# Kernel optimization log

Measured on AMD Instinct MI355X. Metric: run time of the kernel, lower is better.

## Reference

```python
import jax, jax.numpy as jnp
import numpy as np

EMB = 256
N = 262144
B = 512
SLOPE = 0.01  # torch LeakyReLU default negative slope


def leaky_relu(x):
    return jnp.where(x >= 0, x, SLOPE * x)


def setup_inputs() -> dict:
    key = jax.random.key(0)
    ks = jax.random.split(key, 10)
    s = 1.0 / np.sqrt(EMB)
    s2 = 1.0 / np.sqrt(2 * EMB)
    return {
        "xg_prev": jax.random.normal(ks[0], (B, EMB), jnp.float32),
        "x": jax.random.normal(ks[1], (N, EMB), jnp.float32),
        "batch_ind": jnp.sort(jax.random.randint(ks[2], (N,), 0, B)),
        "W_mask": jax.random.uniform(ks[3], (EMB, 1), jnp.float32, -s, s),
        "b_mask": jax.random.uniform(ks[4], (1,), jnp.float32, -s, s),
        "W_feat": jax.random.uniform(ks[5], (EMB, EMB), jnp.float32, -s, s),
        "b_feat": jax.random.uniform(ks[6], (EMB,), jnp.float32, -s, s),
        "W_t": jax.random.uniform(ks[7], (2 * EMB, EMB), jnp.float32, -s2, s2),
        "b_t": jax.random.uniform(ks[8], (EMB,), jnp.float32, -s2, s2),
    }


def reference(xg_prev, x, batch_ind, W_mask, b_mask, W_feat, b_feat, W_t, b_t):
    # GlobalAttention pooling (PyG): gate = att_mask(x), feat = att_feat(x)
    gate = (x @ W_mask + b_mask)[:, 0]                      # [N]
    feat = leaky_relu(x @ W_feat + b_feat)                  # [N, EMB]
    # segment-wise stable softmax over gate per graph
    seg_max = jax.ops.segment_max(gate, batch_ind, num_segments=B)  # [B]
    seg_max = jnp.where(jnp.isfinite(seg_max), seg_max, 0.0)
    e = jnp.exp(gate - seg_max[batch_ind])                  # [N]
    denom = jax.ops.segment_sum(e, batch_ind, num_segments=B)      # [B]
    w = e / jnp.maximum(denom[batch_ind], 1e-16)            # [N]
    xg = jax.ops.segment_sum(w[:, None] * feat, batch_ind, num_segments=B)  # [B, EMB]
    # concat -> linear -> leaky_relu -> residual
    h = jnp.concatenate([xg, xg_prev], axis=1)              # [B, 2*EMB]
    out = leaky_relu(h @ W_t + b_t) + xg_prev               # [B, EMB]
    return out
```

## Files before the change

### kernel.cpp

```cpp
#include <hip/hip_runtime.h>
#include <cstdint>
#include <cstddef>

#define NROWS 262144
#define EMB 256
#define NB 512
#define NCOPY 8
#define SLOPE 0.01f

typedef __attribute__((ext_vector_type(8))) short short8;
typedef __attribute__((ext_vector_type(4))) float f32x4;

__device__ __forceinline__ unsigned short f2bf(float f) {
    unsigned u = __float_as_uint(f);
    u += 0x7FFFu + ((u >> 16) & 1u);
    return (unsigned short)(u >> 16);
}

__device__ __forceinline__ short8 pack8(const float4& lo, const float4& hi) {
    short8 s;
    s[0] = (short)f2bf(lo.x); s[1] = (short)f2bf(lo.y);
    s[2] = (short)f2bf(lo.z); s[3] = (short)f2bf(lo.w);
    s[4] = (short)f2bf(hi.x); s[5] = (short)f2bf(hi.y);
    s[6] = (short)f2bf(hi.z); s[7] = (short)f2bf(hi.w);
    return s;
}

__device__ __forceinline__ void gld16u(unsigned short* l, const unsigned short* g) {
    __builtin_amdgcn_global_load_lds(
        (const __attribute__((address_space(1))) unsigned int*)g,
        (__attribute__((address_space(3))) unsigned int*)l, 16, 0, 0);
}

__global__ __launch_bounds__(256) void k_init(float4* xgPart4, float4* dPart4) {
    int i = blockIdx.x * 256 + threadIdx.x;
    if (i < NCOPY * NB * EMB / 4) xgPart4[i] = (float4){0.f, 0.f, 0.f, 0.f};
    else dPart4[i - NCOPY * NB * EMB / 4] = (float4){0.f, 0.f, 0.f, 0.f};
}

__global__ __launch_bounds__(256) void k_prep(const float* __restrict__ Wf,
                                              unsigned short* __restrict__ Wt2) {
    int b = blockIdx.x, t = threadIdx.x;
    float v = Wf[(size_t)b * EMB + t];
    Wt2[((size_t)(b >> 3) << 11) + (t << 3) + (b & 7)] = f2bf(v);
}

#define STAGE_B(B, KT) do {                                                       \
    _Pragma("unroll")                                                             \
    for (int q = 0; q < 2; q++) {                                                 \
        const int i_ = q * 512 + t;                                               \
        const int slab_ = i_ >> 8, off_ = i_ & 255;                               \
        gld16u(&bbuf[B][slab_ * 2048 + off_ * 8],                                 \
               Wt2 + (((size_t)((KT) >> 3) + slab_) << 11) + off_ * 8);           \
    }                                                                             \
} while (0)

__global__ __launch_bounds__(512, 6) void k_fused(const float* __restrict__ x,
                                                  const unsigned short* __restrict__ Wt2,
                                                  const float* __restrict__ wm,
                                                  const float* __restrict__ bfeat,
                                                  const int* __restrict__ bind,
                                                  float* __restrict__ dPart,
                                                  float* __restrict__ xgPart) {
    __shared__ unsigned short bbuf[2][32 * 256];
    __shared__ float wm_s[256];
    __shared__ float w_s[64];
    __shared__ float pxg[2][256];
    __shared__ float pden[2];
    __shared__ int   seg_s[64];
    __shared__ int   segid_s[4];
    __shared__ int   uni_s[4];

    const int t    = threadIdx.x;
    const int lane = t & 63;
    const int w    = t >> 6;
    const int wr   = w >> 1, wc = w & 1;
    const int fr   = lane & 15;
    const int fg   = lane >> 4;
    const size_t r0 = (size_t)blockIdx.x * 64;
    const int cp   = blockIdx.x & (NCOPY - 1);

    if (t < 256) { wm_s[t] = wm[t]; pxg[0][t] = 0.f; pxg[1][t] = 0.f; }
    if (t < 64) seg_s[t] = bind[r0 + t];
    if (t < 2)  pden[t] = 0.f;

    const float* xrow = x + (r0 + wr * 16 + fr) * EMB + fg * 8;

    STAGE_B(0, 0);
    float4 aLo = *reinterpret_cast<const float4*>(xrow);
    float4 aHi = *reinterpret_cast<const float4*>(xrow + 4);

    f32x4 acc[8];
#pragma unroll
    for (int n = 0; n < 8; n++) acc[n] = (f32x4){0.f, 0.f, 0.f, 0.f};
    float gp = 0.f;

#pragma unroll
    for (int s = 0; s < 8; s++) {
        const int buf = s & 1;
        float4 nLo, nHi;
        if (s < 7) {
            STAGE_B(buf ^ 1, (s + 1) * 32);
            nLo = *reinterpret_cast<const float4*>(xrow + (s + 1) * 32);
            nHi = *reinterpret_cast<const float4*>(xrow + (s + 1) * 32 + 4);
        }
        if (s < 7) asm volatile("s_waitcnt vmcnt(6)" ::: "memory");
        else       asm volatile("s_waitcnt vmcnt(0)" ::: "memory");
        __builtin_amdgcn_sched_barrier(0);
        __builtin_amdgcn_s_barrier();
        __builtin_amdgcn_sched_barrier(0);

        const float4 wa  = *reinterpret_cast<const float4*>(&wm_s[s * 32 + fg * 8]);
        const float4 wbv = *reinterpret_cast<const float4*>(&wm_s[s * 32 + fg * 8 + 4]);
        gp += aLo.x * wa.x + aLo.y * wa.y + aLo.z * wa.z + aLo.w * wa.w
            + aHi.x * wbv.x + aHi.y * wbv.y + aHi.z * wbv.z + aHi.w * wbv.w;
        const short8 a = pack8(aLo, aHi);
        const unsigned short* bb = &bbuf[buf][0];
#pragma unroll
        for (int n = 0; n < 8; n++) {
            const short8 b = *reinterpret_cast<const short8*>(
                &bb[fg * 2048 + ((wc * 128 + n * 16 + fr) << 3)]);
            acc[n] = __builtin_amdgcn_mfma_f32_16x16x32_bf16(a, b, acc[n], 0, 0, 0);
        }

        asm volatile("s_waitcnt lgkmcnt(0)" ::: "memory");
        __builtin_amdgcn_sched_barrier(0);
        __builtin_amdgcn_s_barrier();
        __builtin_amdgcn_sched_barrier(0);

        aLo = nLo; aHi = nHi;
    }

    gp += __shfl_xor(gp, 16, 64);
    gp += __shfl_xor(gp, 32, 64);
    if (wc == 0 && lane < 16) w_s[wr * 16 + lane] = expf(gp);
    if (t < 4) {
        int s0 = seg_s[t * 16], ok = 1;
#pragma unroll
        for (int i = 1; i < 16; i++) ok &= (seg_s[t * 16 + i] == s0);
        segid_s[t] = s0;
        uni_s[t]   = ok;
    }
    __syncthreads();

    const int sid0 = seg_s[0];
    const int sid1 = seg_s[63];

    if (t < 4) {
        if (uni_s[t]) {
            float s = 0.f;
#pragma unroll
            for (int i = 0; i < 16; i++) s += w_s[t * 16 + i];
            const int sid = segid_s[t];
            if (sid == sid0)      atomicAdd(&pden[0], s);
            else if (sid == sid1) atomicAdd(&pden[1], s);
            else atomicAdd(&dPart[cp * NB + sid], s);
        } else {
            for (int i = 0; i < 16; i++) {
                const int sd = seg_s[t * 16 + i];
                const float e = w_s[t * 16 + i];
                if (sd == sid0)      atomicAdd(&pden[0], e);
                else if (sd == sid1) atomicAdd(&pden[1], e);
                else atomicAdd(&dPart[cp * NB + sd], e);
            }
        }
    }

    {
        const int g    = wr;
        const int uni  = uni_s[g];
        const int sid  = segid_s[g];
        const int rowb = wr * 16;
#pragma unroll
        for (int n = 0; n < 8; n++) {
            const int col = wc * 128 + n * 16 + fr;
            const float bia = bfeat[col];
            float vr[4];
#pragma unroll
            for (int r = 0; r < 4; r++) {
                const int row = rowb + fg * 4 + r;
                float v = acc[n][r] + bia;
                v = (v >= 0.f) ? v : SLOPE * v;
                vr[r] = v * w_s[row];
            }
            if (uni) {
                float s = vr[0] + vr[1] + vr[2] + vr[3];
                s += __shfl_xor(s, 16, 64);
                s += __shfl_xor(s, 32, 64);
                if (fg == 0) {
                    if (sid == sid0)      atomicAdd(&pxg[0][col], s);
                    else if (sid == sid1) atomicAdd(&pxg[1][col], s);
                    else atomicAdd(&xgPart[((size_t)(cp * NB + sid) << 8) + col], s);
                }
            } else {
#pragma unroll
                for (int r = 0; r < 4; r++) {
                    const int sd = seg_s[rowb + fg * 4 + r];
                    if (sd == sid0)      atomicAdd(&pxg[0][col], vr[r]);
                    else if (sd == sid1) atomicAdd(&pxg[1][col], vr[r]);
                    else atomicAdd(&xgPart[((size_t)(cp * NB + sd) << 8) + col], vr[r]);
                }
            }
        }
    }
    __syncthreads();

    if (t < 256) {
        atomicAdd(&xgPart[((size_t)(cp * NB + sid0) << 8) + t], pxg[0][t]);
    } else if (sid1 != sid0) {
        atomicAdd(&xgPart[((size_t)(cp * NB + sid1) << 8) + (t - 256)], pxg[1][t - 256]);
    }
    if (t == 0) atomicAdd(&dPart[cp * NB + sid0], pden[0]);
    if (t == 1 && sid1 != sid0) atomicAdd(&dPart[cp * NB + sid1], pden[1]);
}

__global__ __launch_bounds__(256) void k_out(const float* __restrict__ xgPart,
                                             const float* __restrict__ dPart,
                                             const float* __restrict__ xgp,
                                             const float* __restrict__ Wtr,
                                             const float* __restrict__ bt,
                                             float* __restrict__ out) {
    __shared__ float h[8][512];
    const int c  = threadIdx.x;
    const int b0 = blockIdx.x * 8;
#pragma unroll
    for (int r = 0; r < 8; r++) {
        const int b = b0 + r;
        float den = 0.f, s = 0.f;
#pragma unroll
        for (int cpy = 0; cpy < NCOPY; cpy++) {
            den += dPart[cpy * NB + b];
            s   += xgPart[((size_t)(cpy * NB + b) << 8) + c];
        }
        h[r][c]       = s / fmaxf(den, 1e-16f);
        h[r][EMB + c] = xgp[(size_t)b * EMB + c];
    }
    __syncthreads();
    float acc[8] = {0.f, 0.f, 0.f, 0.f, 0.f, 0.f, 0.f, 0.f};
    for (int k = 0; k < 2 * EMB; k++) {
        float wv = Wtr[(size_t)k * EMB + c];
#pragma unroll
        for (int r = 0; r < 8; r++) acc[r] += h[r][k] * wv;
    }
#pragma unroll
    for (int r = 0; r < 8; r++) {
        float v = acc[r] + bt[c];
        v = (v >= 0.f) ? v : SLOPE * v;
        out[(size_t)(b0 + r) * EMB + c] = v + xgp[(size_t)(b0 + r) * EMB + c];
    }
}

extern "C" void kernel_launch(void* const* d_in, const int* in_sizes, int n_in,
                              void* d_out, int out_size, void* d_ws, size_t ws_size,
                              hipStream_t stream) {
    const float* xgp  = (const float*)d_in[0];
    const float* x    = (const float*)d_in[1];
    const int*   bind = (const int*)d_in[2];
    const float* Wm   = (const float*)d_in[3];
    const float* Wf   = (const float*)d_in[5];
    const float* bf   = (const float*)d_in[6];
    const float* Wtr  = (const float*)d_in[7];
    const float* bt   = (const float*)d_in[8];
    float* out = (float*)d_out;

    char* ws = (char*)d_ws;
    unsigned short* Wt2    = (unsigned short*)ws;
    float*          dPart  = (float*)(ws + 131072);
    float*          xgPart = (float*)(ws + 131072 + 16384);

    hipLaunchKernelGGL(k_init,  dim3(1028),       dim3(256), 0, stream,
                       (float4*)xgPart, (float4*)dPart);
    hipLaunchKernelGGL(k_prep,  dim3(256),        dim3(256), 0, stream, Wf, Wt2);
    hipLaunchKernelGGL(k_fused, dim3(NROWS / 64), dim3(512), 0, stream,
                       x, Wt2, Wm, bf, bind, dPart, xgPart);
    hipLaunchKernelGGL(k_out,   dim3(NB / 8),     dim3(256), 0, stream,
                       xgPart, dPart, xgp, Wtr, bt, out);
}
```

Before: 161.3 us.

## Stage x tiles into LDS via async global_load_lds and merge init into prep

The main kernel now loads x through async global-to-LDS copies into a double-buffered, XOR-swizzled shared tile instead of direct register loads. Each thread then reads its A fragment from LDS. This is meant to overlap x loads with MFMA work and cut VGPR pressure. It costs 16KB of extra LDS per block, which may lower occupancy. Separately, the zeroing kernel is folded into the weight-prep kernel to save one launch.

```diff
diff --git a/kernel.cpp b/kernel.cpp
--- a/kernel.cpp
+++ b/kernel.cpp
@@ -26,26 +26,38 @@
     return s;
 }
 
+__device__ __forceinline__ void gld16f(float* l, const float* g) {
+    __builtin_amdgcn_global_load_lds(
+        (const __attribute__((address_space(1))) unsigned int*)g,
+        (__attribute__((address_space(3))) unsigned int*)l, 16, 0, 0);
+}
 __device__ __forceinline__ void gld16u(unsigned short* l, const unsigned short* g) {
     __builtin_amdgcn_global_load_lds(
         (const __attribute__((address_space(1))) unsigned int*)g,
         (__attribute__((address_space(3))) unsigned int*)l, 16, 0, 0);
 }
 
-__global__ __launch_bounds__(256) void k_init(float4* xgPart4, float4* dPart4) {
-    int i = blockIdx.x * 256 + threadIdx.x;
-    if (i < NCOPY * NB * EMB / 4) xgPart4[i] = (float4){0.f, 0.f, 0.f, 0.f};
-    else dPart4[i - NCOPY * NB * EMB / 4] = (float4){0.f, 0.f, 0.f, 0.f};
-}
-
 __global__ __launch_bounds__(256) void k_prep(const float* __restrict__ Wf,
-                                              unsigned short* __restrict__ Wt2) {
-    int b = blockIdx.x, t = threadIdx.x;
-    float v = Wf[(size_t)b * EMB + t];
-    Wt2[((size_t)(b >> 3) << 11) + (t << 3) + (b & 7)] = f2bf(v);
-}
-
-#define STAGE_B(B, KT) do {                                                       \
+                                              unsigned short* __restrict__ Wt2,
+                                              float4* __restrict__ xgPart4,
+                                              float4* __restrict__ dPart4) {
+    const int b = blockIdx.x, t = threadIdx.x;
+    if (b < 256) {
+        float v = Wf[(size_t)b * EMB + t];
+        Wt2[((size_t)(b >> 3) << 11) + (t << 3) + (b & 7)] = f2bf(v);
+    } else {
+        const int i = (b - 256) * 256 + t;
+        if (i < NCOPY * NB * EMB / 4) xgPart4[i] = (float4){0.f, 0.f, 0.f, 0.f};
+        else dPart4[i - NCOPY * NB * EMB / 4] = (float4){0.f, 0.f, 0.f, 0.f};
+    }
+}
+
+#define STAGE(B, KT) do {                                                         \
+    {                                                                             \
+        const int row_ = t >> 3, c_ = t & 7;                                      \
+        const int cs_ = c_ ^ (row_ & 7);                                          \
+        gld16f(&xbuf[B][t * 4], x + ((r0 + row_) << 8) + (KT) + (cs_ << 2));      \
+    }                                                                             \
     _Pragma("unroll")                                                             \
     for (int q = 0; q < 2; q++) {                                                 \
         const int i_ = q * 512 + t;                                               \
@@ -62,6 +74,7 @@
                                                   const int* __restrict__ bind,
                                                   float* __restrict__ dPart,
                                                   float* __restrict__ xgPart) {
+    __shared__ float          xbuf[2][64 * 32];
     __shared__ unsigned short bbuf[2][32 * 256];
     __shared__ float wm_s[256];
     __shared__ float w_s[64];
@@ -84,11 +97,7 @@
     if (t < 64) seg_s[t] = bind[r0 + t];
     if (t < 2)  pden[t] = 0.f;
 
-    const float* xrow = x + (r0 + wr * 16 + fr) * EMB + fg * 8;
-
-    STAGE_B(0, 0);
-    float4 aLo = *reinterpret_cast<const float4*>(xrow);
-    float4 aHi = *reinterpret_cast<const float4*>(xrow + 4);
+    STAGE(0, 0);
 
     f32x4 acc[8];
 #pragma unroll
@@ -98,24 +107,26 @@
 #pragma unroll
     for (int s = 0; s < 8; s++) {
         const int buf = s & 1;
-        float4 nLo, nHi;
-        if (s < 7) {
-            STAGE_B(buf ^ 1, (s + 1) * 32);
-            nLo = *reinterpret_cast<const float4*>(xrow + (s + 1) * 32);
-            nHi = *reinterpret_cast<const float4*>(xrow + (s + 1) * 32 + 4);
-        }
-        if (s < 7) asm volatile("s_waitcnt vmcnt(6)" ::: "memory");
-        else       asm volatile("s_waitcnt vmcnt(0)" ::: "memory");
+        if (s < 7) STAGE(buf ^ 1, (s + 1) * 32);
+        if (s == 0)     asm volatile("s_waitcnt vmcnt(3) lgkmcnt(0)" ::: "memory");
+        else if (s < 7) asm volatile("s_waitcnt vmcnt(3)" ::: "memory");
+        else            asm volatile("s_waitcnt vmcnt(0)" ::: "memory");
         __builtin_amdgcn_sched_barrier(0);
         __builtin_amdgcn_s_barrier();
         __builtin_amdgcn_sched_barrier(0);
+
+        const float* xb = &xbuf[buf][0];
+        const unsigned short* bb = &bbuf[buf][0];
 
         const float4 wa  = *reinterpret_cast<const float4*>(&wm_s[s * 32 + fg * 8]);
         const float4 wbv = *reinterpret_cast<const float4*>(&wm_s[s * 32 + fg * 8 + 4]);
-        gp += aLo.x * wa.x + aLo.y * wa.y + aLo.z * wa.z + aLo.w * wa.w
-            + aHi.x * wbv.x + aHi.y * wbv.y + aHi.z * wbv.z + aHi.w * wbv.w;
-        const short8 a = pack8(aLo, aHi);
-        const unsigned short* bb = &bbuf[buf][0];
+        const int r  = wr * 16 + fr;
+        const int sl = (fg * 2) ^ (r & 7);
+        const float4 lo = *reinterpret_cast<const float4*>(&xb[r * 32 + sl * 4]);
+        const float4 hi = *reinterpret_cast<const float4*>(&xb[r * 32 + (sl ^ 1) * 4]);
+        gp += lo.x * wa.x + lo.y * wa.y + lo.z * wa.z + lo.w * wa.w
+            + hi.x * wbv.x + hi.y * wbv.y + hi.z * wbv.z + hi.w * wbv.w;
+        const short8 a = pack8(lo, hi);
 #pragma unroll
         for (int n = 0; n < 8; n++) {
             const short8 b = *reinterpret_cast<const short8*>(
@@ -127,8 +138,6 @@
         __builtin_amdgcn_sched_barrier(0);
         __builtin_amdgcn_s_barrier();
         __builtin_amdgcn_sched_barrier(0);
-
-        aLo = nLo; aHi = nHi;
     }
 
     gp += __shfl_xor(gp, 16, 64);
@@ -167,9 +176,8 @@
     }
 
     {
-        const int g    = wr;
-        const int uni  = uni_s[g];
-        const int sid  = segid_s[g];
+        const int uni  = uni_s[wr];
+        const int sid  = segid_s[wr];
         const int rowb = wr * 16;
 #pragma unroll
         for (int n = 0; n < 8; n++) {
@@ -177,11 +185,11 @@
             const float bia = bfeat[col];
             float vr[4];
 #pragma unroll
-            for (int r = 0; r < 4; r++) {
-                const int row = rowb + fg * 4 + r;
-                float v = acc[n][r] + bia;
+            for (int r2 = 0; r2 < 4; r2++) {
+                const int row = rowb + fg * 4 + r2;
+                float v = acc[n][r2] + bia;
                 v = (v >= 0.f) ? v : SLOPE * v;
-                vr[r] = v * w_s[row];
+                vr[r2] = v * w_s[row];
             }
             if (uni) {
                 float s = vr[0] + vr[1] + vr[2] + vr[3];
@@ -194,11 +202,11 @@
                 }
             } else {
 #pragma unroll
-                for (int r = 0; r < 4; r++) {
-                    const int sd = seg_s[rowb + fg * 4 + r];
-                    if (sd == sid0)      atomicAdd(&pxg[0][col], vr[r]);
-                    else if (sd == sid1) atomicAdd(&pxg[1][col], vr[r]);
-                    else atomicAdd(&xgPart[((size_t)(cp * NB + sd) << 8) + col], vr[r]);
+                for (int r2 = 0; r2 < 4; r2++) {
+                    const int sd = seg_s[rowb + fg * 4 + r2];
+                    if (sd == sid0)      atomicAdd(&pxg[0][col], vr[r2]);
+                    else if (sd == sid1) atomicAdd(&pxg[1][col], vr[r2]);
+                    else atomicAdd(&xgPart[((size_t)(cp * NB + sd) << 8) + col], vr[r2]);
                 }
             }
         }
@@ -268,9 +276,8 @@
     float*          dPart  = (float*)(ws + 131072);
     float*          xgPart = (float*)(ws + 131072 + 16384);
 
-    hipLaunchKernelGGL(k_init,  dim3(1028),       dim3(256), 0, stream,
-                       (float4*)xgPart, (float4*)dPart);
-    hipLaunchKernelGGL(k_prep,  dim3(256),        dim3(256), 0, stream, Wf, Wt2);
+    hipLaunchKernelGGL(k_prep,  dim3(256 + 1028), dim3(256), 0, stream,
+                       Wf, Wt2, (float4*)xgPart, (float4*)dPart);
     hipLaunchKernelGGL(k_fused, dim3(NROWS / 64), dim3(512), 0, stream,
                        x, Wt2, Wm, bf, bind, dPart, xgPart);
     hipLaunchKernelGGL(k_out,   dim3(NB / 8),     dim3(256), 0, stream,
```

Result: faster. 149.5 us (-7.3%).
